# Optimization experiments

Hardware: AMD Instinct MI355X
Metric: run time of the kernel (lower is better)

## Reference

```python
import jax, jax.numpy as jnp
import numpy as np

B, S, D_MODEL, N_HEADS, D_K, D_V = 4, 1024, 1024, 16, 64, 64


def setup_inputs() -> dict:
    key = jax.random.key(0)
    ks = jax.random.split(key, 12)
    s = 1.0 / np.sqrt(D_MODEL)
    inp = {
        'Q': jax.random.normal(ks[0], (B, S, D_MODEL), jnp.float32),
        'K': jax.random.normal(ks[1], (B, S, D_MODEL), jnp.float32),
        'V': jax.random.normal(ks[2], (B, S, D_MODEL), jnp.float32),
        'attn_mask': jax.random.randint(ks[3], (B, S, S), 0, 2) == 1,
        'Wq': jax.random.normal(ks[4], (D_MODEL, N_HEADS * D_K), jnp.float32) * s,
        'bq': jnp.zeros((N_HEADS * D_K,), jnp.float32),
        'Wk': jax.random.normal(ks[5], (D_MODEL, N_HEADS * D_K), jnp.float32) * s,
        'bk': jnp.zeros((N_HEADS * D_K,), jnp.float32),
        'Wv': jax.random.normal(ks[6], (D_MODEL, N_HEADS * D_V), jnp.float32) * s,
        'bv': jnp.zeros((N_HEADS * D_V,), jnp.float32),
        'Wo': jax.random.normal(ks[7], (N_HEADS * D_V, D_MODEL), jnp.float32) * s,
        'bo': jnp.zeros((D_MODEL,), jnp.float32),
        'gamma': jnp.ones((D_MODEL,), jnp.float32),
        'beta': jnp.zeros((D_MODEL,), jnp.float32),
    }
    return inp


def reference(Q, K, V, attn_mask, Wq, bq, Wk, bk, Wv, bv, Wo, bo, gamma, beta):
    # QKV projections -> [B, H, S, d]
    q = (Q @ Wq + bq).reshape(B, S, N_HEADS, D_K).transpose(0, 2, 1, 3)
    k = (K @ Wk + bk).reshape(B, S, N_HEADS, D_K).transpose(0, 2, 1, 3)
    v = (V @ Wv + bv).reshape(B, S, N_HEADS, D_V).transpose(0, 2, 1, 3)
    # scaled dot-product attention with explicit mask (masked_fill with -1e9)
    scores = jnp.einsum('bhqd,bhkd->bhqk', q, k) / np.sqrt(D_K)
    scores = jnp.where(attn_mask[:, None, :, :], -1e9, scores)
    attn = jax.nn.softmax(scores, axis=-1)
    context = jnp.einsum('bhqk,bhkd->bhqd', attn, v)
    context = context.transpose(0, 2, 1, 3).reshape(B, S, N_HEADS * D_V)
    # output projection + residual + LayerNorm(d_model)
    y = context @ Wo + bo + Q
    mean = jnp.mean(y, axis=-1, keepdims=True)
    var = jnp.var(y, axis=-1, keepdims=True)
    out = (y - mean) / jnp.sqrt(var + 1e-5) * gamma + beta
    return out, attn
```

## Files before the change

kernel.cpp:

```cpp
#include <hip/hip_runtime.h>

constexpr int NB = 4;
constexpr int SQ = 1024;
constexpr int DM = 1024;
constexpr int NH = 16;
constexpr int DK = 64;

typedef __attribute__((ext_vector_type(8))) __bf16 bf16x8;
typedef __attribute__((ext_vector_type(4))) float f32x4;

#define MFMA16(a, b, c) __builtin_amdgcn_mfma_f32_16x16x32_bf16((a), (b), (c), 0, 0, 0)

__device__ __forceinline__ short f2bf(float f) {
    unsigned u = __float_as_uint(f);
    unsigned r = 0x7fffu + ((u >> 16) & 1u);
    return (short)((u + r) >> 16);
}

__device__ __forceinline__ int4 pack_bf16x8(float4 a, float4 b) {
    union { short s[8]; int4 v; } u;
    u.s[0] = f2bf(a.x); u.s[1] = f2bf(a.y); u.s[2] = f2bf(a.z); u.s[3] = f2bf(a.w);
    u.s[4] = f2bf(b.x); u.s[5] = f2bf(b.y); u.s[6] = f2bf(b.z); u.s[7] = f2bf(b.w);
    return u.v;
}

__global__ __launch_bounds__(256) void maskpack_kernel(
    const int* __restrict__ mask, unsigned long long* __restrict__ mpk)
{
    const int wid  = (blockIdx.x * 256 + threadIdx.x) >> 6;
    const int lane = threadIdx.x & 63;
    const int nw   = (gridDim.x * 256) >> 6;
    const int nwords = NB * SQ * SQ / 64;
    for (int w = wid; w < nwords; w += nw) {
        int v = mask[(size_t)w * 64 + lane];
        unsigned long long b = __ballot(v != 0);
        if (lane == 0) mpk[w] = b;
    }
}

__global__ __launch_bounds__(256) void wtrans_kernel(
    const float* __restrict__ W0, const float* __restrict__ W1,
    const float* __restrict__ W2, const float* __restrict__ W3,
    short* __restrict__ T0, short* __restrict__ T1,
    short* __restrict__ T2, short* __restrict__ T3)
{
    const int z = blockIdx.z;
    const float* W = (z == 0) ? W0 : (z == 1) ? W1 : (z == 2) ? W2 : W3;
    short* T       = (z == 0) ? T0 : (z == 1) ? T1 : (z == 2) ? T2 : T3;
    __shared__ float tile[32][33];
    const int n0 = blockIdx.x * 32, k0 = blockIdx.y * 32;
    const int c = threadIdx.x & 31, r0 = threadIdx.x >> 5;
#pragma unroll
    for (int i = 0; i < 4; i++) {
        int r = r0 + i * 8;
        tile[r][c] = W[(size_t)(k0 + r) * DM + n0 + c];
    }
    __syncthreads();
#pragma unroll
    for (int i = 0; i < 4; i++) {
        int r = r0 + i * 8;
        T[(size_t)(n0 + r) * DM + k0 + c] = f2bf(tile[c][r]);
    }
}

template<int MODE, bool CVTA>
__device__ __forceinline__ void gemm_core(
    const void* __restrict__ Av, const short* __restrict__ BT,
    const float* __restrict__ bias, const float* __restrict__ resid,
    short* __restrict__ obf, float* __restrict__ of)
{
    __shared__ short As[128][40];
    __shared__ short Bs[128][40];
    __shared__ short Cs[128 * 72];

    const int t = threadIdx.x;
    const int m0 = blockIdx.y * 128, n0 = blockIdx.x * 128;
    const int w = t >> 6, lane = t & 63, quad = lane >> 4, l16 = lane & 15;
    const int wm = (w & 1) * 64, wn = (w >> 1) * 64;
    const int srow = t >> 2, sseg = (t & 3) * 8;
    const float* Af = (const float*)Av;
    const short* Ab = (const short*)Av;

    const f32x4 fz = {0.f, 0.f, 0.f, 0.f};
    f32x4 acc[4][4];
#pragma unroll
    for (int i = 0; i < 4; i++)
#pragma unroll
        for (int j = 0; j < 4; j++) acc[i][j] = fz;

    auto ldA = [&](int k0, int off) -> int4 {
        if constexpr (CVTA) {
            const float* p = &Af[(size_t)(m0 + off + srow) * DM + k0 + sseg];
            float4 f0 = *(const float4*)p;
            float4 f1 = *(const float4*)(p + 4);
            return pack_bf16x8(f0, f1);
        } else {
            return *(const int4*)&Ab[(size_t)(m0 + off + srow) * DM + k0 + sseg];
        }
    };
    auto ldB = [&](int k0, int off) -> int4 {
        return *(const int4*)&BT[(size_t)(n0 + off + srow) * DM + k0 + sseg];
    };

    int4 ra0 = ldA(0, 0), ra1 = ldA(0, 64);
    int4 rb0 = ldB(0, 0), rb1 = ldB(0, 64);

    for (int k0 = 0; k0 < DM; k0 += 32) {
        __syncthreads();
        *(int4*)&As[srow][sseg] = ra0;
        *(int4*)&As[64 + srow][sseg] = ra1;
        *(int4*)&Bs[srow][sseg] = rb0;
        *(int4*)&Bs[64 + srow][sseg] = rb1;
        __syncthreads();
        if (k0 + 32 < DM) {
            ra0 = ldA(k0 + 32, 0); ra1 = ldA(k0 + 32, 64);
            rb0 = ldB(k0 + 32, 0); rb1 = ldB(k0 + 32, 64);
        }
        bf16x8 af[4], bfr[4];
#pragma unroll
        for (int mi = 0; mi < 4; mi++)
            af[mi] = *(const bf16x8*)&As[wm + mi * 16 + l16][quad * 8];
#pragma unroll
        for (int ni = 0; ni < 4; ni++)
            bfr[ni] = *(const bf16x8*)&Bs[wn + ni * 16 + l16][quad * 8];
#pragma unroll
        for (int mi = 0; mi < 4; mi++)
#pragma unroll
            for (int ni = 0; ni < 4; ni++)
                acc[mi][ni] = MFMA16(af[mi], bfr[ni], acc[mi][ni]);
    }

    if constexpr (MODE == 2) {
#pragma unroll
        for (int ni = 0; ni < 4; ni++) {
            const int col = n0 + wn + ni * 16 + l16;
            const float bb = bias[col];
#pragma unroll
            for (int mi = 0; mi < 4; mi++) {
#pragma unroll
                for (int r = 0; r < 4; r++) {
                    const int row = m0 + wm + mi * 16 + quad * 4 + r;
                    of[(size_t)row * DM + col] =
                        acc[mi][ni][r] + bb + resid[(size_t)row * DM + col];
                }
            }
        }
    } else {
        for (int hf = 0; hf < 2; hf++) {
            __syncthreads();
            if ((w >> 1) == hf) {
#pragma unroll
                for (int ni = 0; ni < 4; ni++) {
                    const int cl = ni * 16 + l16;
                    const float bb = bias[n0 + hf * 64 + cl];
#pragma unroll
                    for (int mi = 0; mi < 4; mi++)
#pragma unroll
                        for (int r = 0; r < 4; r++) {
                            const int row = wm + mi * 16 + quad * 4 + r;
                            short v = f2bf(acc[mi][ni][r] + bb);
                            if (MODE == 0) Cs[row * 72 + cl] = v;
                            else           Cs[cl * 136 + row] = v;
                        }
                }
            }
            __syncthreads();
            const int hh = (n0 >> 6) + hf;
            if (MODE == 0) {
                const int row = t >> 1, sg = (t & 1) * 32;
                const int gr = m0 + row, bi = gr >> 10, s = gr & 1023;
                const short* src = &Cs[row * 72 + sg];
                short* dst = &obf[(((size_t)(bi * NH + hh)) * SQ + s) * DK + sg];
#pragma unroll
                for (int k = 0; k < 4; k++)
                    *(int4*)&dst[k * 8] = *(const int4*)&src[k * 8];
            } else {
                const int dd = t >> 2, off = (t & 3) * 32;
                const int bi = m0 >> 10;
                const short* src = &Cs[dd * 136 + off];
                short* dst = &obf[(((size_t)(bi * NH + hh)) * DK + dd) * SQ +
                                  (m0 & 1023) + off];
#pragma unroll
                for (int k = 0; k < 4; k++)
                    *(int4*)&dst[k * 8] = *(const int4*)&src[k * 8];
            }
        }
    }
}

__global__ __launch_bounds__(256) void gemm_qkv_kernel(
    const float* __restrict__ Qin, const float* __restrict__ Kin,
    const float* __restrict__ Vin,
    const short* __restrict__ WqT, const short* __restrict__ WkT,
    const short* __restrict__ WvT,
    const float* __restrict__ bq, const float* __restrict__ bk,
    const float* __restrict__ bv,
    short* __restrict__ q_ws, short* __restrict__ k_ws,
    short* __restrict__ vt_ws)
{
    const int z = blockIdx.z;
    if (z == 0)      gemm_core<0, true>(Qin, WqT, bq, nullptr, q_ws, nullptr);
    else if (z == 1) gemm_core<0, true>(Kin, WkT, bk, nullptr, k_ws, nullptr);
    else             gemm_core<1, true>(Vin, WvT, bv, nullptr, vt_ws, nullptr);
}

__global__ __launch_bounds__(256) void gemm_out_kernel(
    const short* __restrict__ ctx, const short* __restrict__ WoT,
    const float* __restrict__ bo, const float* __restrict__ resid,
    float* __restrict__ y)
{
    gemm_core<2, false>(ctx, WoT, bo, resid, nullptr, y);
}

__global__ __launch_bounds__(256) void attn_kernel(
    const short* __restrict__ q_ws, const short* __restrict__ k_ws,
    const short* __restrict__ vt_ws, const unsigned* __restrict__ mpk,
    float* __restrict__ attn, short* __restrict__ ctx)
{
    __shared__ short Ps[4][16][136];

    const int t = threadIdx.x, w = t >> 6, lane = t & 63;
    const int quad = lane >> 4, l16 = lane & 15;
    const int qt = blockIdx.x, h = blockIdx.y, b = blockIdx.z;
    const size_t bh = (size_t)b * NH + h;
    const short* qb  = q_ws + (bh * SQ + qt * 64) * DK;
    const short* kb  = k_ws + bh * SQ * DK;
    const short* vtb = vt_ws + bh * DK * SQ;
    const unsigned* mrow = mpk + ((size_t)b * SQ + qt * 64) * 32;
    float* attnb = attn + (bh * SQ + (size_t)qt * 64) * SQ;
    const int lqb = w * 16 + quad * 4;

    const bf16x8 aq0 = *(const bf16x8*)&qb[(w * 16 + l16) * DK + quad * 8];
    const bf16x8 aq1 = *(const bf16x8*)&qb[(w * 16 + l16) * DK + 32 + quad * 8];
    const f32x4 fz = {0.f, 0.f, 0.f, 0.f};

    float lsum[4] = {0.f, 0.f, 0.f, 0.f};
    for (int ch = 0; ch < 8; ch++) {
        uint4 mw[4];
#pragma unroll
        for (int r = 0; r < 4; r++)
            mw[r] = *(const uint4*)&mrow[(lqb + r) * 32 + ch * 4];
#pragma unroll
        for (int nt = 0; nt < 8; nt++) {
            const short* kp = &kb[(size_t)(ch * 128 + nt * 16 + l16) * DK + quad * 8];
            bf16x8 b0 = *(const bf16x8*)kp;
            bf16x8 b1 = *(const bf16x8*)(kp + 32);
            f32x4 a = fz;
            a = MFMA16(aq0, b0, a);
            a = MFMA16(aq1, b1, a);
#pragma unroll
            for (int r = 0; r < 4; r++) {
                unsigned wd = ((const unsigned*)&mw[r])[nt >> 1];
                unsigned bit = (wd >> ((nt & 1) * 16 + l16)) & 1u;
                float p = bit ? 0.f : __expf(a[r] * 0.125f);
                lsum[r] += p;
            }
        }
    }
    float inv[4];
#pragma unroll
    for (int r = 0; r < 4; r++) {
#pragma unroll
        for (int off = 1; off < 16; off <<= 1)
            lsum[r] += __shfl_xor(lsum[r], off, 64);
        inv[r] = 1.f / (lsum[r] + 1e-30f);
    }

    f32x4 Oacc[4] = {fz, fz, fz, fz};
    for (int ch = 0; ch < 8; ch++) {
        uint4 mw[4];
#pragma unroll
        for (int r = 0; r < 4; r++)
            mw[r] = *(const uint4*)&mrow[(lqb + r) * 32 + ch * 4];
        __syncthreads();
#pragma unroll
        for (int nt = 0; nt < 8; nt++) {
            const short* kp = &kb[(size_t)(ch * 128 + nt * 16 + l16) * DK + quad * 8];
            bf16x8 b0 = *(const bf16x8*)kp;
            bf16x8 b1 = *(const bf16x8*)(kp + 32);
            f32x4 a = fz;
            a = MFMA16(aq0, b0, a);
            a = MFMA16(aq1, b1, a);
            const int key = ch * 128 + nt * 16 + l16;
#pragma unroll
            for (int r = 0; r < 4; r++) {
                unsigned wd = ((const unsigned*)&mw[r])[nt >> 1];
                unsigned bit = (wd >> ((nt & 1) * 16 + l16)) & 1u;
                float p = bit ? 0.f : __expf(a[r] * 0.125f) * inv[r];
                attnb[(size_t)(lqb + r) * SQ + key] = p;
                Ps[w][quad * 4 + r][nt * 16 + l16] = f2bf(p);
            }
        }
        __syncthreads();
#pragma unroll
        for (int ks = 0; ks < 4; ks++) {
            bf16x8 ap = *(const bf16x8*)&Ps[w][l16][ks * 32 + quad * 8];
#pragma unroll
            for (int dt = 0; dt < 4; dt++) {
                bf16x8 bv = *(const bf16x8*)
                    &vtb[(size_t)(dt * 16 + l16) * SQ + ch * 128 + ks * 32 + quad * 8];
                Oacc[dt] = MFMA16(ap, bv, Oacc[dt]);
            }
        }
    }

#pragma unroll
    for (int dt = 0; dt < 4; dt++) {
        const int col = h * DK + dt * 16 + l16;
#pragma unroll
        for (int r = 0; r < 4; r++)
            ctx[((size_t)b * SQ + qt * 64 + lqb + r) * DM + col] = f2bf(Oacc[dt][r]);
    }
}

__global__ __launch_bounds__(256) void ln_kernel(
    const float* __restrict__ y, const float* __restrict__ gamma,
    const float* __restrict__ beta, float* __restrict__ out)
{
    const int r = blockIdx.x;
    const int t = threadIdx.x;
    float4 v = *(const float4*)&y[(size_t)r * DM + t * 4];
    float s  = v.x + v.y + v.z + v.w;
    float sq = v.x * v.x + v.y * v.y + v.z * v.z + v.w * v.w;
#pragma unroll
    for (int off = 32; off > 0; off >>= 1) {
        s  += __shfl_xor(s, off, 64);
        sq += __shfl_xor(sq, off, 64);
    }
    __shared__ float rs[4], rq[4];
    const int lane = t & 63, w = t >> 6;
    if (lane == 0) { rs[w] = s; rq[w] = sq; }
    __syncthreads();
    s  = rs[0] + rs[1] + rs[2] + rs[3];
    sq = rq[0] + rq[1] + rq[2] + rq[3];
    const float mean = s * (1.f / 1024.f);
    const float var  = sq * (1.f / 1024.f) - mean * mean;
    const float rstd = rsqrtf(var + 1e-5f);
    float4 g  = *(const float4*)&gamma[t * 4];
    float4 be = *(const float4*)&beta[t * 4];
    float4 o;
    o.x = (v.x - mean) * rstd * g.x + be.x;
    o.y = (v.y - mean) * rstd * g.y + be.y;
    o.z = (v.z - mean) * rstd * g.z + be.z;
    o.w = (v.w - mean) * rstd * g.w + be.w;
    *(float4*)&out[(size_t)r * DM + t * 4] = o;
}

extern "C" void kernel_launch(void* const* d_in, const int* in_sizes, int n_in,
                              void* d_out, int out_size, void* d_ws, size_t ws_size,
                              hipStream_t stream)
{
    const float* Q     = (const float*)d_in[0];
    const float* Kin   = (const float*)d_in[1];
    const float* Vin   = (const float*)d_in[2];
    const int*   mask  = (const int*)d_in[3];
    const float* Wq    = (const float*)d_in[4];
    const float* bq    = (const float*)d_in[5];
    const float* Wk    = (const float*)d_in[6];
    const float* bk    = (const float*)d_in[7];
    const float* Wv    = (const float*)d_in[8];
    const float* bv    = (const float*)d_in[9];
    const float* Wo    = (const float*)d_in[10];
    const float* bo    = (const float*)d_in[11];
    const float* gamma = (const float*)d_in[12];
    const float* beta  = (const float*)d_in[13];

    float* out  = (float*)d_out;
    float* attn = out + (size_t)NB * SQ * DM;

    const size_t NE = (size_t)NB * SQ * DM;
    const size_t WE = (size_t)DM * DM;
    short* wsb   = (short*)d_ws;
    short* WqT   = wsb;
    short* WkT   = WqT + WE;
    short* WvT   = WkT + WE;
    short* WoT   = WvT + WE;
    short* q_ws  = WoT + WE;
    short* k_ws  = q_ws + NE;
    short* vt_ws = k_ws + NE;
    short* ctx   = vt_ws + NE;
    unsigned* mpk = (unsigned*)(ctx + NE);
    float* y = (float*)q_ws;

    maskpack_kernel<<<dim3(256), 256, 0, stream>>>(
        mask, (unsigned long long*)mpk);
    wtrans_kernel<<<dim3(32, 32, 4), 256, 0, stream>>>(
        Wq, Wk, Wv, Wo, WqT, WkT, WvT, WoT);

    gemm_qkv_kernel<<<dim3(8, 32, 3), 256, 0, stream>>>(
        Q, Kin, Vin, WqT, WkT, WvT, bq, bk, bv, q_ws, k_ws, vt_ws);

    attn_kernel<<<dim3(16, 16, 4), 256, 0, stream>>>(
        q_ws, k_ws, vt_ws, mpk, attn, ctx);

    gemm_out_kernel<<<dim3(8, 32, 1), 256, 0, stream>>>(ctx, WoT, bo, Q, y);

    ln_kernel<<<NB * SQ, 256, 0, stream>>>(y, gamma, beta, out);
}
```

Measured before the change: 698.1 us.

## Split attention keys across waves, shrink LDS tile, swizzle block order

Result: faster. 671.3 us (-3.8%).

```diff
diff --git a/kernel.cpp b/kernel.cpp
--- a/kernel.cpp
+++ b/kernel.cpp
@@ -217,25 +217,32 @@
     const short* __restrict__ vt_ws, const unsigned* __restrict__ mpk,
     float* __restrict__ attn, short* __restrict__ ctx)
 {
-    __shared__ short Ps[4][16][136];
+    __shared__ short Ps[4][16][40];
+    __shared__ float Lx[4][4][4];
+    __shared__ float Ox[2][64][16];
 
     const int t = threadIdx.x, w = t >> 6, lane = t & 63;
     const int quad = lane >> 4, l16 = lane & 15;
-    const int qt = blockIdx.x, h = blockIdx.y, b = blockIdx.z;
+    const int qg = w & 1, kh = w >> 1;
+    const int wgid = blockIdx.x;
+    const int bh_i = (wgid & 7) + ((wgid >> 8) << 3);
+    const int qt   = (wgid >> 3) & 31;
+    const int h = bh_i & 15, b = bh_i >> 4;
     const size_t bh = (size_t)b * NH + h;
-    const short* qb  = q_ws + (bh * SQ + qt * 64) * DK;
-    const short* kb  = k_ws + bh * SQ * DK;
+    const int qrow0 = qt * 32 + qg * 16;
+    const short* qb  = q_ws + (bh * SQ + qrow0) * DK;
+    const short* kb  = k_ws + bh * SQ * DK + (size_t)kh * 512 * DK;
     const short* vtb = vt_ws + bh * DK * SQ;
-    const unsigned* mrow = mpk + ((size_t)b * SQ + qt * 64) * 32;
-    float* attnb = attn + (bh * SQ + (size_t)qt * 64) * SQ;
-    const int lqb = w * 16 + quad * 4;
-
-    const bf16x8 aq0 = *(const bf16x8*)&qb[(w * 16 + l16) * DK + quad * 8];
-    const bf16x8 aq1 = *(const bf16x8*)&qb[(w * 16 + l16) * DK + 32 + quad * 8];
+    const unsigned* mrow = mpk + ((size_t)b * SQ + qrow0) * 32 + kh * 16;
+    float* attnb = attn + (bh * SQ + (size_t)qrow0) * SQ + kh * 512;
+    const int lqb = quad * 4;
+
+    const bf16x8 aq0 = *(const bf16x8*)&qb[l16 * DK + quad * 8];
+    const bf16x8 aq1 = *(const bf16x8*)&qb[l16 * DK + 32 + quad * 8];
     const f32x4 fz = {0.f, 0.f, 0.f, 0.f};
 
     float lsum[4] = {0.f, 0.f, 0.f, 0.f};
-    for (int ch = 0; ch < 8; ch++) {
+    for (int ch = 0; ch < 4; ch++) {
         uint4 mw[4];
 #pragma unroll
         for (int r = 0; r < 4; r++)
@@ -257,59 +264,79 @@
             }
         }
     }
-    float inv[4];
-#pragma unroll
-    for (int r = 0; r < 4; r++) {
+#pragma unroll
+    for (int r = 0; r < 4; r++)
 #pragma unroll
         for (int off = 1; off < 16; off <<= 1)
             lsum[r] += __shfl_xor(lsum[r], off, 64);
-        inv[r] = 1.f / (lsum[r] + 1e-30f);
-    }
+    if (l16 == 0) {
+#pragma unroll
+        for (int r = 0; r < 4; r++) Lx[w][quad][r] = lsum[r];
+    }
+    __syncthreads();
+    float inv[4];
+#pragma unroll
+    for (int r = 0; r < 4; r++)
+        inv[r] = 1.f / (lsum[r] + Lx[w ^ 2][quad][r] + 1e-30f);
 
     f32x4 Oacc[4] = {fz, fz, fz, fz};
-    for (int ch = 0; ch < 8; ch++) {
+    for (int ch = 0; ch < 4; ch++) {
         uint4 mw[4];
 #pragma unroll
         for (int r = 0; r < 4; r++)
             mw[r] = *(const uint4*)&mrow[(lqb + r) * 32 + ch * 4];
-        __syncthreads();
-#pragma unroll
-        for (int nt = 0; nt < 8; nt++) {
-            const short* kp = &kb[(size_t)(ch * 128 + nt * 16 + l16) * DK + quad * 8];
-            bf16x8 b0 = *(const bf16x8*)kp;
-            bf16x8 b1 = *(const bf16x8*)(kp + 32);
-            f32x4 a = fz;
-            a = MFMA16(aq0, b0, a);
-            a = MFMA16(aq1, b1, a);
-            const int key = ch * 128 + nt * 16 + l16;
-#pragma unroll
-            for (int r = 0; r < 4; r++) {
-                unsigned wd = ((const unsigned*)&mw[r])[nt >> 1];
-                unsigned bit = (wd >> ((nt & 1) * 16 + l16)) & 1u;
-                float p = bit ? 0.f : __expf(a[r] * 0.125f) * inv[r];
-                attnb[(size_t)(lqb + r) * SQ + key] = p;
-                Ps[w][quad * 4 + r][nt * 16 + l16] = f2bf(p);
-            }
-        }
-        __syncthreads();
 #pragma unroll
         for (int ks = 0; ks < 4; ks++) {
-            bf16x8 ap = *(const bf16x8*)&Ps[w][l16][ks * 32 + quad * 8];
+#pragma unroll
+            for (int ntp = 0; ntp < 2; ntp++) {
+                const int nt = ks * 2 + ntp;
+                const short* kp = &kb[(size_t)(ch * 128 + nt * 16 + l16) * DK + quad * 8];
+                bf16x8 b0 = *(const bf16x8*)kp;
+                bf16x8 b1 = *(const bf16x8*)(kp + 32);
+                f32x4 a = fz;
+                a = MFMA16(aq0, b0, a);
+                a = MFMA16(aq1, b1, a);
+                float pv[4];
+#pragma unroll
+                for (int r = 0; r < 4; r++) {
+                    unsigned wd = ((const unsigned*)&mw[r])[nt >> 1];
+                    unsigned bit = (wd >> ((nt & 1) * 16 + l16)) & 1u;
+                    pv[r] = bit ? 0.f : __expf(a[r] * 0.125f) * inv[r];
+                    Ps[w][lqb + r][ntp * 16 + l16] = f2bf(pv[r]);
+                }
+                const int key = ch * 128 + nt * 16 + l16;
+#pragma unroll
+                for (int r = 0; r < 4; r++)
+                    attnb[(size_t)(lqb + r) * SQ + key] = pv[r];
+            }
+            bf16x8 ap = *(const bf16x8*)&Ps[w][l16][quad * 8];
 #pragma unroll
             for (int dt = 0; dt < 4; dt++) {
                 bf16x8 bv = *(const bf16x8*)
-                    &vtb[(size_t)(dt * 16 + l16) * SQ + ch * 128 + ks * 32 + quad * 8];
+                    &vtb[(size_t)(dt * 16 + l16) * SQ + kh * 512 + ch * 128 + ks * 32 + quad * 8];
                 Oacc[dt] = MFMA16(ap, bv, Oacc[dt]);
             }
         }
     }
 
-#pragma unroll
-    for (int dt = 0; dt < 4; dt++) {
-        const int col = h * DK + dt * 16 + l16;
-#pragma unroll
-        for (int r = 0; r < 4; r++)
-            ctx[((size_t)b * SQ + qt * 64 + lqb + r) * DM + col] = f2bf(Oacc[dt][r]);
+    if (kh == 1) {
+#pragma unroll
+        for (int dt = 0; dt < 4; dt++)
+#pragma unroll
+            for (int r = 0; r < 4; r++)
+                Ox[qg][lane][dt * 4 + r] = Oacc[dt][r];
+    }
+    __syncthreads();
+    if (kh == 0) {
+#pragma unroll
+        for (int dt = 0; dt < 4; dt++) {
+            const int col = h * DK + dt * 16 + l16;
+#pragma unroll
+            for (int r = 0; r < 4; r++) {
+                float o = Oacc[dt][r] + Ox[qg][lane][dt * 4 + r];
+                ctx[((size_t)b * SQ + qrow0 + lqb + r) * DM + col] = f2bf(o);
+            }
+        }
     }
 }
 
@@ -390,7 +417,7 @@
     gemm_qkv_kernel<<<dim3(8, 32, 3), 256, 0, stream>>>(
         Q, Kin, Vin, WqT, WkT, WvT, bq, bk, bv, q_ws, k_ws, vt_ws);
 
-    attn_kernel<<<dim3(16, 16, 4), 256, 0, stream>>>(
+    attn_kernel<<<dim3(2048), 256, 0, stream>>>(
         q_ws, k_ws, vt_ws, mpk, attn, ctx);
 
     gemm_out_kernel<<<dim3(8, 32, 1), 256, 0, stream>>>(ctx, WoT, bo, Q, y);
```

## Single-pass attention with split-key waves, deferred normalization, and vectorized attn stores

Applied to the files above, without the earlier changes.

Result: faster. 617.7 us (-11.5%).

```diff
diff --git a/kernel.cpp b/kernel.cpp
--- a/kernel.cpp
+++ b/kernel.cpp
@@ -15,6 +15,10 @@
     unsigned u = __float_as_uint(f);
     unsigned r = 0x7fffu + ((u >> 16) & 1u);
     return (short)((u + r) >> 16);
+}
+
+__device__ __forceinline__ float bf2f(short s) {
+    return __uint_as_float(((unsigned)(unsigned short)s) << 16);
 }
 
 __device__ __forceinline__ int4 pack_bf16x8(float4 a, float4 b) {
@@ -212,104 +216,121 @@
     gemm_core<2, false>(ctx, WoT, bo, resid, nullptr, y);
 }
 
-__global__ __launch_bounds__(256) void attn_kernel(
+__global__ __launch_bounds__(256, 4) void attn_kernel(
     const short* __restrict__ q_ws, const short* __restrict__ k_ws,
     const short* __restrict__ vt_ws, const unsigned* __restrict__ mpk,
     float* __restrict__ attn, short* __restrict__ ctx)
 {
-    __shared__ short Ps[4][16][136];
+    __shared__ short Ps[4][16][264];
+    __shared__ float Lx[4][16];
 
     const int t = threadIdx.x, w = t >> 6, lane = t & 63;
     const int quad = lane >> 4, l16 = lane & 15;
-    const int qt = blockIdx.x, h = blockIdx.y, b = blockIdx.z;
+    const int kh = w;
+    const int wgid = blockIdx.x;
+    const int bh_i = (wgid & 7) + ((wgid >> 9) << 3);
+    const int qt   = (wgid >> 3) & 63;
+    const int h = bh_i & 15, b = bh_i >> 4;
     const size_t bh = (size_t)b * NH + h;
-    const short* qb  = q_ws + (bh * SQ + qt * 64) * DK;
-    const short* kb  = k_ws + bh * SQ * DK;
+    const int qrow0 = qt * 16;
+    const short* qb  = q_ws + (bh * SQ + qrow0) * DK;
+    const short* kb  = k_ws + bh * SQ * DK + (size_t)kh * 256 * DK;
     const short* vtb = vt_ws + bh * DK * SQ;
-    const unsigned* mrow = mpk + ((size_t)b * SQ + qt * 64) * 32;
-    float* attnb = attn + (bh * SQ + (size_t)qt * 64) * SQ;
-    const int lqb = w * 16 + quad * 4;
-
-    const bf16x8 aq0 = *(const bf16x8*)&qb[(w * 16 + l16) * DK + quad * 8];
-    const bf16x8 aq1 = *(const bf16x8*)&qb[(w * 16 + l16) * DK + 32 + quad * 8];
+    const unsigned* mrow = mpk + ((size_t)b * SQ + qrow0) * 32 + kh * 8;
+    float* attnb = attn + (bh * SQ + (size_t)qrow0) * SQ + kh * 256;
+
+    const bf16x8 aq0 = *(const bf16x8*)&qb[l16 * DK + quad * 8];
+    const bf16x8 aq1 = *(const bf16x8*)&qb[l16 * DK + 32 + quad * 8];
     const f32x4 fz = {0.f, 0.f, 0.f, 0.f};
 
-    float lsum[4] = {0.f, 0.f, 0.f, 0.f};
-    for (int ch = 0; ch < 8; ch++) {
-        uint4 mw[4];
-#pragma unroll
-        for (int r = 0; r < 4; r++)
-            mw[r] = *(const uint4*)&mrow[(lqb + r) * 32 + ch * 4];
-#pragma unroll
-        for (int nt = 0; nt < 8; nt++) {
-            const short* kp = &kb[(size_t)(ch * 128 + nt * 16 + l16) * DK + quad * 8];
-            bf16x8 b0 = *(const bf16x8*)kp;
-            bf16x8 b1 = *(const bf16x8*)(kp + 32);
-            f32x4 a = fz;
-            a = MFMA16(aq0, b0, a);
-            a = MFMA16(aq1, b1, a);
-#pragma unroll
-            for (int r = 0; r < 4; r++) {
-                unsigned wd = ((const unsigned*)&mw[r])[nt >> 1];
-                unsigned bit = (wd >> ((nt & 1) * 16 + l16)) & 1u;
-                float p = bit ? 0.f : __expf(a[r] * 0.125f);
-                lsum[r] += p;
-            }
-        }
-    }
-    float inv[4];
-#pragma unroll
-    for (int r = 0; r < 4; r++) {
-#pragma unroll
-        for (int off = 1; off < 16; off <<= 1)
-            lsum[r] += __shfl_xor(lsum[r], off, 64);
-        inv[r] = 1.f / (lsum[r] + 1e-30f);
-    }
-
+    float lsum = 0.f;
     f32x4 Oacc[4] = {fz, fz, fz, fz};
-    for (int ch = 0; ch < 8; ch++) {
-        uint4 mw[4];
-#pragma unroll
-        for (int r = 0; r < 4; r++)
-            mw[r] = *(const uint4*)&mrow[(lqb + r) * 32 + ch * 4];
-        __syncthreads();
-#pragma unroll
-        for (int nt = 0; nt < 8; nt++) {
-            const short* kp = &kb[(size_t)(ch * 128 + nt * 16 + l16) * DK + quad * 8];
-            bf16x8 b0 = *(const bf16x8*)kp;
-            bf16x8 b1 = *(const bf16x8*)(kp + 32);
-            f32x4 a = fz;
-            a = MFMA16(aq0, b0, a);
-            a = MFMA16(aq1, b1, a);
-            const int key = ch * 128 + nt * 16 + l16;
-#pragma unroll
-            for (int r = 0; r < 4; r++) {
-                unsigned wd = ((const unsigned*)&mw[r])[nt >> 1];
-                unsigned bit = (wd >> ((nt & 1) * 16 + l16)) & 1u;
-                float p = bit ? 0.f : __expf(a[r] * 0.125f) * inv[r];
-                attnb[(size_t)(lqb + r) * SQ + key] = p;
-                Ps[w][quad * 4 + r][nt * 16 + l16] = f2bf(p);
-            }
-        }
-        __syncthreads();
+
+    for (int ch = 0; ch < 2; ch++) {
+        const uint4 mw = *(const uint4*)&mrow[l16 * 32 + ch * 4];
 #pragma unroll
         for (int ks = 0; ks < 4; ks++) {
-            bf16x8 ap = *(const bf16x8*)&Ps[w][l16][ks * 32 + quad * 8];
+#pragma unroll
+            for (int ntp = 0; ntp < 2; ntp++) {
+                const int nt = ks * 2 + ntp;
+                const short* kp = &kb[(size_t)(ch * 128 + nt * 16 + l16) * DK + quad * 8];
+                bf16x8 k0 = *(const bf16x8*)kp;
+                bf16x8 k1 = *(const bf16x8*)(kp + 32);
+                f32x4 a = fz;
+                a = MFMA16(k0, aq0, a);
+                a = MFMA16(k1, aq1, a);
+                const unsigned wd = ((const unsigned*)&mw)[nt >> 1];
+                union { short s[4]; uint2 v; } pb;
+#pragma unroll
+                for (int r = 0; r < 4; r++) {
+                    unsigned bit = (wd >> ((nt & 1) * 16 + quad * 4 + r)) & 1u;
+                    float p = bit ? 0.f : __expf(a[r] * 0.125f);
+                    lsum += p;
+                    pb.s[r] = f2bf(p);
+                }
+                *(uint2*)&Ps[w][l16][ch * 128 + nt * 16 + quad * 4] = pb.v;
+            }
+            bf16x8 ap = *(const bf16x8*)&Ps[w][l16][ch * 128 + ks * 32 + quad * 8];
 #pragma unroll
             for (int dt = 0; dt < 4; dt++) {
                 bf16x8 bv = *(const bf16x8*)
-                    &vtb[(size_t)(dt * 16 + l16) * SQ + ch * 128 + ks * 32 + quad * 8];
+                    &vtb[(size_t)(dt * 16 + l16) * SQ + kh * 256 + ch * 128 + ks * 32 + quad * 8];
                 Oacc[dt] = MFMA16(ap, bv, Oacc[dt]);
             }
         }
     }
 
-#pragma unroll
-    for (int dt = 0; dt < 4; dt++) {
-        const int col = h * DK + dt * 16 + l16;
-#pragma unroll
-        for (int r = 0; r < 4; r++)
-            ctx[((size_t)b * SQ + qt * 64 + lqb + r) * DM + col] = f2bf(Oacc[dt][r]);
+    lsum += __shfl_xor(lsum, 16, 64);
+    lsum += __shfl_xor(lsum, 32, 64);
+    if (lane < 16) Lx[w][lane] = lsum;
+    __syncthreads();
+    const float invL =
+        1.f / (Lx[0][l16] + Lx[1][l16] + Lx[2][l16] + Lx[3][l16] + 1e-30f);
+
+#pragma unroll
+    for (int j = 0; j < 8; j++) {
+        union { int4 v; short s[8]; } u;
+        u.v = *(const int4*)&Ps[w][l16][j * 32 + quad * 8];
+        float4 o0, o1;
+        o0.x = bf2f(u.s[0]) * invL; o0.y = bf2f(u.s[1]) * invL;
+        o0.z = bf2f(u.s[2]) * invL; o0.w = bf2f(u.s[3]) * invL;
+        o1.x = bf2f(u.s[4]) * invL; o1.y = bf2f(u.s[5]) * invL;
+        o1.z = bf2f(u.s[6]) * invL; o1.w = bf2f(u.s[7]) * invL;
+        float* dst = &attnb[(size_t)l16 * SQ + j * 32 + quad * 8];
+        *(float4*)dst = o0;
+        *(float4*)(dst + 4) = o1;
+    }
+    __syncthreads();
+
+    float* Oxp = (float*)&Ps[0][0][0];
+    if (kh != 0) {
+#pragma unroll
+        for (int dt = 0; dt < 4; dt++)
+#pragma unroll
+            for (int r = 0; r < 4; r++)
+                Oxp[((kh - 1) * 64 + lane) * 16 + dt * 4 + r] = Oacc[dt][r];
+    }
+    __syncthreads();
+    if (kh == 0) {
+        float invq[4];
+#pragma unroll
+        for (int r = 0; r < 4; r++) {
+            const int qr = quad * 4 + r;
+            invq[r] = 1.f / (Lx[0][qr] + Lx[1][qr] + Lx[2][qr] + Lx[3][qr] + 1e-30f);
+        }
+#pragma unroll
+        for (int dt = 0; dt < 4; dt++) {
+            const int col = h * DK + dt * 16 + l16;
+#pragma unroll
+            for (int r = 0; r < 4; r++) {
+                float o = Oacc[dt][r];
+#pragma unroll
+                for (int kk = 0; kk < 3; kk++)
+                    o += Oxp[(kk * 64 + lane) * 16 + dt * 4 + r];
+                ctx[((size_t)b * SQ + qrow0 + quad * 4 + r) * DM + col] =
+                    f2bf(o * invq[r]);
+            }
+        }
     }
 }
 
@@ -390,7 +411,7 @@
     gemm_qkv_kernel<<<dim3(8, 32, 3), 256, 0, stream>>>(
         Q, Kin, Vin, WqT, WkT, WvT, bq, bk, bv, q_ws, k_ws, vt_ws);
 
-    attn_kernel<<<dim3(16, 16, 4), 256, 0, stream>>>(
+    attn_kernel<<<dim3(4096), 256, 0, stream>>>(
         q_ws, k_ws, vt_ws, mpk, attn, ctx);
 
     gemm_out_kernel<<<dim3(8, 32, 1), 256, 0, stream>>>(ctx, WoT, bo, Q, y);
```
